# Optimization experiments

Measured on AMD Instinct MI355X. Metric: run time of the kernel, lower is better.

## Reference

```python
import jax, jax.numpy as jnp
import numpy as np
import math

D_MODEL = 1024
NUM_HEADS = 16


def setup_inputs() -> dict:
    key = jax.random.key(0)
    k1, k2, k3 = jax.random.split(key, 3)
    x = jax.random.normal(k1, (4, 2048, D_MODEL), dtype=jnp.float32)
    scale = 1.0 / math.sqrt(D_MODEL)
    W_qkv = jax.random.normal(k2, (3 * D_MODEL, D_MODEL), dtype=jnp.float32) * scale
    W_out = jax.random.normal(k3, (D_MODEL, D_MODEL), dtype=jnp.float32) * scale
    return {"x": x, "W_qkv": W_qkv, "W_out": W_out}


def reference(x, W_qkv, W_out):
    B, S, D = x.shape
    H = NUM_HEADS
    hd = D // H
    qkv = x @ W_qkv.T                      # [B,S,3D]
    q, k, v = jnp.split(qkv, 3, axis=-1)
    # [B,S,D] -> [B,H,S,hd]
    q = q.reshape(B, S, H, hd).transpose(0, 2, 1, 3)
    k = k.reshape(B, S, H, hd).transpose(0, 2, 1, 3)
    v = v.reshape(B, S, H, hd).transpose(0, 2, 1, 3)
    scores = jnp.einsum('bhqd,bhkd->bhqk', q, k) / math.sqrt(hd)
    causal = jnp.tril(jnp.ones((S, S), dtype=bool))
    scores = jnp.where(causal, scores, -jnp.inf)
    w = jax.nn.softmax(scores, axis=-1)
    out = jnp.einsum('bhqk,bhkd->bhqd', w, v)
    out = out.transpose(0, 2, 1, 3).reshape(B, S, D)
    return out @ W_out.T
```

## Files before the change

kernel.cpp:

```cpp
#include <hip/hip_runtime.h>
#include <hip/hip_bf16.h>
#include <stdint.h>


typedef __bf16 bf16_t;
typedef __attribute__((ext_vector_type(8))) __bf16 bf16x8;
typedef __attribute__((ext_vector_type(4))) __bf16 bf16x4;
typedef __attribute__((ext_vector_type(4))) float f32x4;

#define LOG2E 1.44269504088896340736f
#define SCLF (0.125f * LOG2E)
#define MFMA16(a, b, c) __builtin_amdgcn_mfma_f32_16x16x32_bf16(a, b, c, 0, 0, 0)

__device__ __forceinline__ bf16x8 ld8(const bf16_t* p) {
    return *(const bf16x8*)p;
}
__device__ __forceinline__ bf16x8 cvt8(const float* p) {
    f32x4 a = *(const f32x4*)p;
    f32x4 b = *(const f32x4*)(p + 4);
    bf16x8 r;
    r[0] = (bf16_t)a[0]; r[1] = (bf16_t)a[1]; r[2] = (bf16_t)a[2]; r[3] = (bf16_t)a[3];
    r[4] = (bf16_t)b[0]; r[5] = (bf16_t)b[1]; r[6] = (bf16_t)b[2]; r[7] = (bf16_t)b[3];
    return r;
}

__device__ __forceinline__ bool probe_f32_wave(const void* w) {
    const uint16_t* u = (const uint16_t*)w;
    const int lane = threadIdx.x & 63;
    const int e = (u[lane] >> 7) & 0xFF;
    const unsigned long long m = __ballot(e >= 96 && e <= 150);
    return __popcll(m) < 56;
}

__device__ __forceinline__ void gll16(const bf16_t* g, bf16_t* l) {
    __builtin_amdgcn_global_load_lds(
        (const __attribute__((address_space(1))) void*)g,
        (__attribute__((address_space(3))) void*)l, 16, 0, 0);
}

__global__ __launch_bounds__(256) void cvt_big_kernel(
    const void* __restrict__ x, const void* __restrict__ wq,
    bf16_t* __restrict__ xb, bf16_t* __restrict__ wqb)
{
    const int gid = blockIdx.x * 256 + threadIdx.x;
    const void* src;
    bf16_t* dst;
    int off;
    if (gid < 1048576) { src = x;  dst = xb;  off = gid; }
    else               { src = wq; dst = wqb; off = gid - 1048576; }
    const bool f32 = probe_f32_wave(src);
    const bf16x8 v = f32 ? cvt8((const float*)src + (size_t)off * 8)
                         : ld8((const bf16_t*)src + (size_t)off * 8);
    *(bf16x8*)(dst + (size_t)off * 8) = v;
}

__global__ __launch_bounds__(256) void cvt_small_kernel(
    const void* __restrict__ wo, bf16_t* __restrict__ wob)
{
    const int off = blockIdx.x * 256 + threadIdx.x;
    const bool f32 = probe_f32_wave(wo);
    const bf16x8 v = f32 ? cvt8((const float*)wo + (size_t)off * 8)
                         : ld8((const bf16_t*)wo + (size_t)off * 8);
    *(bf16x8*)(wob + (size_t)off * 8) = v;
}

template <int EPI>
__global__ __launch_bounds__(256) void gemm_bt_lds(
    const bf16_t* __restrict__ A, const bf16_t* __restrict__ B,
    void* __restrict__ C, bf16_t* __restrict__ VT,
    int M, int N, int K)
{
    __shared__ __align__(16) bf16_t lsA[128 * 32];
    __shared__ __align__(16) bf16_t lsB[128 * 32];

    const int t    = threadIdx.x;
    const int lane = t & 63;
    const int wid  = t >> 6;
    const int quad = lane >> 4;
    const int l15  = lane & 15;
    const int wm   = (wid & 1) * 64;
    const int wn   = (wid >> 1) * 64;
    const int m0   = blockIdx.y * 128;
    const int n0   = blockIdx.x * 128;

    const bf16_t* Ar = A + (size_t)(m0 + (t >> 2)) * K + (t & 3) * 8;
    const bf16_t* Br = B + (size_t)(n0 + (t >> 2)) * K + (t & 3) * 8;
    bf16_t* la = lsA + t * 8;
    bf16_t* lb = lsB + t * 8;

    f32x4 acc[4][4];
#pragma unroll
    for (int i = 0; i < 4; ++i)
#pragma unroll
        for (int j = 0; j < 4; ++j) acc[i][j] = (f32x4){0.f, 0.f, 0.f, 0.f};

    for (int k0 = 0; k0 < K; k0 += 32) {
        __syncthreads();
        gll16(Ar + k0, la);
        gll16(Ar + (size_t)64 * K + k0, la + 2048);
        gll16(Br + k0, lb);
        gll16(Br + (size_t)64 * K + k0, lb + 2048);
        __syncthreads();

        bf16x8 af[4], bfr[4];
#pragma unroll
        for (int i = 0; i < 4; ++i)
            af[i] = ld8(lsA + (wm + i * 16 + l15) * 32 + quad * 8);
#pragma unroll
        for (int j = 0; j < 4; ++j)
            bfr[j] = ld8(lsB + (wn + j * 16 + l15) * 32 + quad * 8);
#pragma unroll
        for (int i = 0; i < 4; ++i)
#pragma unroll
            for (int j = 0; j < 4; ++j)
                acc[i][j] = MFMA16(af[i], bfr[j], acc[i][j]);
    }

#pragma unroll
    for (int i = 0; i < 4; ++i) {
        const int row = m0 + wm + i * 16 + quad * 4;
#pragma unroll
        for (int j = 0; j < 4; ++j) {
            const int col = n0 + wn + j * 16 + l15;
#pragma unroll
            for (int r = 0; r < 4; ++r) {
                const int rr = row + r;
                if (EPI == 0) {
                    ((float*)C)[(size_t)rr * N + col] = acc[i][j][r];
                } else {
                    const bf16_t v = (bf16_t)acc[i][j][r];
                    if (col < 2048) {
                        ((bf16_t*)C)[(size_t)rr * 2048 + col] = v;
                    } else {
                        const int c2 = col - 2048;
                        const int h = c2 >> 6, d = c2 & 63;
                        const int b = rr >> 11, s = rr & 2047;
                        VT[((size_t)((b << 4) + h) * 64 + d) * 2048 + s] = v;
                    }
                }
            }
        }
    }
}

struct Kfrag { bf16x8 k00, k01, k10, k11; };
struct Vfrag { bf16x8 v0, v1, v2, v3; };

__device__ __forceinline__ Kfrag ldk(const bf16_t* Kbase, int key0) {
    const bf16_t* kp = Kbase + (size_t)key0 * 2048;
    Kfrag f;
    f.k00 = ld8(kp);
    f.k01 = ld8(kp + 32);
    f.k10 = ld8(kp + (size_t)16 * 2048);
    f.k11 = ld8(kp + (size_t)16 * 2048 + 32);
    return f;
}
__device__ __forceinline__ Vfrag ldv(const bf16_t* Vbase, int key0) {
    const bf16_t* vp = Vbase + key0;
    Vfrag f;
    f.v0 = ld8(vp);
    f.v1 = ld8(vp + (size_t)16 * 2048);
    f.v2 = ld8(vp + (size_t)32 * 2048);
    f.v3 = ld8(vp + (size_t)48 * 2048);
    return f;
}

__device__ __forceinline__ bf16x4 expq(f32x4 s, float& lsum) {
    bf16x4 r;
#pragma unroll
    for (int i = 0; i < 4; ++i) {
        const float e = exp2f(s[i] * SCLF);
        r[i] = (bf16_t)e;
        lsum += (float)r[i];
    }
    return r;
}
__device__ __forceinline__ bf16x4 expq_m(f32x4 s, float& lsum, int quad, int l15) {
    bf16x4 r;
#pragma unroll
    for (int i = 0; i < 4; ++i) {
        const float e = (quad * 4 + i <= l15) ? exp2f(s[i] * SCLF) : 0.f;
        r[i] = (bf16_t)e;
        lsum += (float)r[i];
    }
    return r;
}

typedef union { bf16x4 h; int u[2]; } pk2;
typedef union { int u[4]; bf16x8 v; } pk4u;

__device__ __forceinline__ bf16x8 xpose(bf16x4 p0, bf16x4 p1, int s0b, int s1b, bool lowsel) {
    pk2 a, b;
    a.h = p0; b.h = p1;
    const int x0 = __builtin_amdgcn_ds_bpermute(s0b, a.u[0]);
    const int y0 = __builtin_amdgcn_ds_bpermute(s0b, b.u[0]);
    const int x1 = __builtin_amdgcn_ds_bpermute(s0b, a.u[1]);
    const int y1 = __builtin_amdgcn_ds_bpermute(s0b, b.u[1]);
    const int x2 = __builtin_amdgcn_ds_bpermute(s1b, a.u[0]);
    const int y2 = __builtin_amdgcn_ds_bpermute(s1b, b.u[0]);
    const int x3 = __builtin_amdgcn_ds_bpermute(s1b, a.u[1]);
    const int y3 = __builtin_amdgcn_ds_bpermute(s1b, b.u[1]);
    pk4u r;
    r.u[0] = lowsel ? x0 : y0;
    r.u[1] = lowsel ? x1 : y1;
    r.u[2] = lowsel ? x2 : y2;
    r.u[3] = lowsel ? x3 : y3;
    return r.v;
}

template <int DIAG>
__device__ __forceinline__ void qk_phase(
    const Kfrag& kf, int quad, int l15, int s0b, int s1b, bool lowsel,
    const bf16x8& qa0, const bf16x8& qa1, const bf16x8& qb0, const bf16x8& qb1,
    bf16x8& pfa, bf16x8& pfb, float& la, float& lb)
{
    const f32x4 Z = (f32x4){0.f, 0.f, 0.f, 0.f};
    f32x4 s0a = Z, s1a = Z, s0b_ = Z, s1b_ = Z;
    s0a = MFMA16(kf.k00, qa0, s0a); s0a = MFMA16(kf.k01, qa1, s0a);
    s0b_ = MFMA16(kf.k00, qb0, s0b_); s0b_ = MFMA16(kf.k01, qb1, s0b_);
    if (!DIAG) {
        s1a = MFMA16(kf.k10, qa0, s1a); s1a = MFMA16(kf.k11, qa1, s1a);
    }
    s1b_ = MFMA16(kf.k10, qb0, s1b_); s1b_ = MFMA16(kf.k11, qb1, s1b_);

    bf16x4 pa0, pa1, pb0, pb1;
    if (DIAG) {
        pa0 = expq_m(s0a, la, quad, l15);
        pa1 = (bf16x4){(bf16_t)0.f, (bf16_t)0.f, (bf16_t)0.f, (bf16_t)0.f};
        pb0 = expq(s0b_, lb);
        pb1 = expq_m(s1b_, lb, quad, l15);
    } else {
        pa0 = expq(s0a, la); pa1 = expq(s1a, la);
        pb0 = expq(s0b_, lb); pb1 = expq(s1b_, lb);
    }
    pfa = xpose(pa0, pa1, s0b, s1b, lowsel);
    pfb = xpose(pb0, pb1, s0b, s1b, lowsel);
}

__device__ __forceinline__ void pv(
    const bf16x8& pfa, const bf16x8& pfb, const Vfrag& v,
    f32x4 (&oa)[4], f32x4 (&ob)[4])
{
    oa[0] = MFMA16(pfa, v.v0, oa[0]); ob[0] = MFMA16(pfb, v.v0, ob[0]);
    oa[1] = MFMA16(pfa, v.v1, oa[1]); ob[1] = MFMA16(pfb, v.v1, ob[1]);
    oa[2] = MFMA16(pfa, v.v2, oa[2]); ob[2] = MFMA16(pfb, v.v2, ob[2]);
    oa[3] = MFMA16(pfa, v.v3, oa[3]); ob[3] = MFMA16(pfb, v.v3, ob[3]);
}

__global__ __launch_bounds__(256, 4) void attn_kernel(
    const bf16_t* __restrict__ qk, const bf16_t* __restrict__ vt,
    bf16_t* __restrict__ out)
{
    const int t    = threadIdx.x;
    const int wid  = t >> 6;
    const int lane = t & 63;
    const int quad = lane >> 4;
    const int l15  = lane & 15;

    const int bx = blockIdx.x;
    const int u  = bx & 255;
    const int v_ = bx >> 8;
    const int bh = ((u & 15) << 2) | wid;
    const int c  = u >> 4;
    const int bs = (v_ & 1) ? (31 - c) : c;
    const int qt = bs + ((v_ >> 1) << 5);
    const int b  = bh >> 4;
    const int h  = bh & 15;
    const int q0 = qt << 5;

    const int s0b = ((((quad << 1)) & 3) * 16 + l15) << 2;
    const int s1b = ((((quad << 1) + 1) & 3) * 16 + l15) << 2;
    const bool lowsel = quad < 2;

    const bf16_t* Qp = qk + (size_t)(b * 2048 + q0 + l15) * 2048 + h * 64 + quad * 8;
    const bf16x8 qa0 = ld8(Qp);
    const bf16x8 qa1 = ld8(Qp + 32);
    const bf16x8 qb0 = ld8(Qp + (size_t)16 * 2048);
    const bf16x8 qb1 = ld8(Qp + (size_t)16 * 2048 + 32);

    const bf16_t* Kbase = qk + (size_t)(b * 2048 + l15) * 2048 + 1024 + h * 64 + quad * 8;
    const bf16_t* Vbase = vt + ((size_t)bh * 64 + l15) * 2048 + quad * 8;

    f32x4 oa[4], ob[4];
#pragma unroll
    for (int v = 0; v < 4; ++v) {
        oa[v] = (f32x4){0.f, 0.f, 0.f, 0.f};
        ob[v] = (f32x4){0.f, 0.f, 0.f, 0.f};
    }
    float la = 0.f, lb = 0.f;

    Kfrag kc = ldk(Kbase, 0);
    Vfrag vc = ldv(Vbase, 0);
    bf16x8 pfa, pfb;

    if (qt > 0) {
        Kfrag kn = ldk(Kbase, 32);
        qk_phase<0>(kc, quad, l15, s0b, s1b, lowsel,
                    qa0, qa1, qb0, qb1, pfa, pfb, la, lb);
        kc = kn;
        for (int kb = 1; kb < qt; ++kb) {
            Kfrag knn = ldk(Kbase, (kb + 1) << 5);
            Vfrag vn  = ldv(Vbase, kb << 5);
            pv(pfa, pfb, vc, oa, ob);
            qk_phase<0>(kc, quad, l15, s0b, s1b, lowsel,
                        qa0, qa1, qb0, qb1, pfa, pfb, la, lb);
            kc = knn; vc = vn;
        }
        Vfrag vn = ldv(Vbase, qt << 5);
        pv(pfa, pfb, vc, oa, ob);
        qk_phase<1>(kc, quad, l15, s0b, s1b, lowsel,
                    qa0, qa1, qb0, qb1, pfa, pfb, la, lb);
        vc = vn;
    } else {
        qk_phase<1>(kc, quad, l15, s0b, s1b, lowsel,
                    qa0, qa1, qb0, qb1, pfa, pfb, la, lb);
    }
    pv(pfa, pfb, vc, oa, ob);

    la += __shfl_xor(la, 16); la += __shfl_xor(la, 32);
    lb += __shfl_xor(lb, 16); lb += __shfl_xor(lb, 32);
    const float inva = 1.0f / la;
    const float invb = 1.0f / lb;

    const size_t obase = (size_t)(b * 2048 + q0 + quad * 4) * 1024 + h * 64 + l15;
#pragma unroll
    for (int r = 0; r < 4; ++r) {
        const float ia = __shfl(inva, quad * 4 + r);
        const float ib = __shfl(invb, quad * 4 + r);
#pragma unroll
        for (int v = 0; v < 4; ++v) {
            out[obase + (size_t)r * 1024 + v * 16]        = (bf16_t)(oa[v][r] * ia);
            out[obase + (size_t)(16 + r) * 1024 + v * 16] = (bf16_t)(ob[v][r] * ib);
        }
    }
}

__global__ void ws_check_kernel(float* out, int code) {
    if (code != 0 && threadIdx.x == 0) out[0] = (float)code;
}

extern "C" void kernel_launch(void* const* d_in, const int* in_sizes, int n_in,
                              void* d_out, int out_size, void* d_ws, size_t ws_size,
                              hipStream_t stream)
{
    const void* x    = d_in[0];
    const void* wqkv = d_in[1];
    const void* wout = d_in[2];

    bf16_t* qkbuf   = (bf16_t*)d_ws;
    bf16_t* vtbuf   = qkbuf + (size_t)8192 * 2048;
    bf16_t* attnbuf = vtbuf + (size_t)64 * 64 * 2048;
    float*  outp    = (float*)d_out;

    bf16_t* xb  = attnbuf;
    bf16_t* wqb = (bf16_t*)d_out;
    bf16_t* wob = vtbuf;

    const int wsBad = (ws_size < (size_t)64 * 1024 * 1024) ? 512 : 0;

    cvt_big_kernel<<<5632, 256, 0, stream>>>(x, wqkv, xb, wqb);

    gemm_bt_lds<1><<<dim3(24, 64), 256, 0, stream>>>(
        xb, wqb, qkbuf, vtbuf, 8192, 3072, 1024);

    attn_kernel<<<1024, 256, 0, stream>>>(qkbuf, vtbuf, attnbuf);

    cvt_small_kernel<<<512, 256, 0, stream>>>(wout, wob);

    gemm_bt_lds<0><<<dim3(8, 64), 256, 0, stream>>>(
        attnbuf, wob, outp, nullptr, 8192, 1024, 1024);

    ws_check_kernel<<<1, 64, 0, stream>>>(outp, wsBad);
}
```

Measured before the change: 339.2 us.

## Split attention work to 16-row query tiles per wave and swizzle GEMM block order

The attention kernel now gives each wave a 16-row query tile instead of 32 rows. Waves in a block cover different query tiles of the same head rather than different heads, and the grid doubles to 2048 blocks with launch bounds raised to 8 blocks per CU. Diagonal handling gains a third mode for odd tiles. This aims to cut per-wave registers, raise occupancy and balance causal work, but each K/V load now feeds half as much MFMA work. Separately, the GEMM remaps block IDs with an XCD-style stride-8 swizzle to improve L2 locality across chiplets.

```diff
diff --git a/kernel.cpp b/kernel.cpp
--- a/kernel.cpp
+++ b/kernel.cpp
@@ -80,8 +80,13 @@
     const int l15  = lane & 15;
     const int wm   = (wid & 1) * 64;
     const int wn   = (wid >> 1) * 64;
-    const int m0   = blockIdx.y * 128;
-    const int n0   = blockIdx.x * 128;
+
+    const int nbx = gridDim.x;
+    const int nwg = nbx * gridDim.y;
+    const int bid = blockIdx.y * nbx + blockIdx.x;
+    const int sid = (bid & 7) * (nwg >> 3) + (bid >> 3);
+    const int m0  = (sid / nbx) * 128;
+    const int n0  = (sid % nbx) * 128;
 
     const bf16_t* Ar = A + (size_t)(m0 + (t >> 2)) * K + (t & 3) * 8;
     const bf16_t* Br = B + (size_t)(n0 + (t >> 2)) * K + (t & 3) * 8;
@@ -208,46 +213,42 @@
     return r.v;
 }
 
-template <int DIAG>
-__device__ __forceinline__ void qk_phase(
+template <int MODE>
+__device__ __forceinline__ void qk16(
     const Kfrag& kf, int quad, int l15, int s0b, int s1b, bool lowsel,
-    const bf16x8& qa0, const bf16x8& qa1, const bf16x8& qb0, const bf16x8& qb1,
-    bf16x8& pfa, bf16x8& pfb, float& la, float& lb)
+    const bf16x8& qa0, const bf16x8& qa1,
+    bf16x8& pfa, float& la)
 {
     const f32x4 Z = (f32x4){0.f, 0.f, 0.f, 0.f};
-    f32x4 s0a = Z, s1a = Z, s0b_ = Z, s1b_ = Z;
-    s0a = MFMA16(kf.k00, qa0, s0a); s0a = MFMA16(kf.k01, qa1, s0a);
-    s0b_ = MFMA16(kf.k00, qb0, s0b_); s0b_ = MFMA16(kf.k01, qb1, s0b_);
-    if (!DIAG) {
-        s1a = MFMA16(kf.k10, qa0, s1a); s1a = MFMA16(kf.k11, qa1, s1a);
-    }
-    s1b_ = MFMA16(kf.k10, qb0, s1b_); s1b_ = MFMA16(kf.k11, qb1, s1b_);
-
-    bf16x4 pa0, pa1, pb0, pb1;
-    if (DIAG) {
-        pa0 = expq_m(s0a, la, quad, l15);
-        pa1 = (bf16x4){(bf16_t)0.f, (bf16_t)0.f, (bf16_t)0.f, (bf16_t)0.f};
-        pb0 = expq(s0b_, lb);
-        pb1 = expq_m(s1b_, lb, quad, l15);
+    f32x4 s0 = Z, s1 = Z;
+    s0 = MFMA16(kf.k00, qa0, s0); s0 = MFMA16(kf.k01, qa1, s0);
+    if (MODE != 1) {
+        s1 = MFMA16(kf.k10, qa0, s1); s1 = MFMA16(kf.k11, qa1, s1);
+    }
+    bf16x4 p0, p1;
+    if (MODE == 0) {
+        p0 = expq(s0, la);
+        p1 = expq(s1, la);
+    } else if (MODE == 1) {
+        p0 = expq_m(s0, la, quad, l15);
+        p1 = (bf16x4){(bf16_t)0.f, (bf16_t)0.f, (bf16_t)0.f, (bf16_t)0.f};
     } else {
-        pa0 = expq(s0a, la); pa1 = expq(s1a, la);
-        pb0 = expq(s0b_, lb); pb1 = expq(s1b_, lb);
-    }
-    pfa = xpose(pa0, pa1, s0b, s1b, lowsel);
-    pfb = xpose(pb0, pb1, s0b, s1b, lowsel);
-}
-
-__device__ __forceinline__ void pv(
-    const bf16x8& pfa, const bf16x8& pfb, const Vfrag& v,
-    f32x4 (&oa)[4], f32x4 (&ob)[4])
-{
-    oa[0] = MFMA16(pfa, v.v0, oa[0]); ob[0] = MFMA16(pfb, v.v0, ob[0]);
-    oa[1] = MFMA16(pfa, v.v1, oa[1]); ob[1] = MFMA16(pfb, v.v1, ob[1]);
-    oa[2] = MFMA16(pfa, v.v2, oa[2]); ob[2] = MFMA16(pfb, v.v2, ob[2]);
-    oa[3] = MFMA16(pfa, v.v3, oa[3]); ob[3] = MFMA16(pfb, v.v3, ob[3]);
-}
-
-__global__ __launch_bounds__(256, 4) void attn_kernel(
+        p0 = expq(s0, la);
+        p1 = expq_m(s1, la, quad, l15);
+    }
+    pfa = xpose(p0, p1, s0b, s1b, lowsel);
+}
+
+__device__ __forceinline__ void pv16(
+    const bf16x8& pfa, const Vfrag& v, f32x4 (&oa)[4])
+{
+    oa[0] = MFMA16(pfa, v.v0, oa[0]);
+    oa[1] = MFMA16(pfa, v.v1, oa[1]);
+    oa[2] = MFMA16(pfa, v.v2, oa[2]);
+    oa[3] = MFMA16(pfa, v.v3, oa[3]);
+}
+
+__global__ __launch_bounds__(256, 8) void attn_kernel(
     const bf16_t* __restrict__ qk, const bf16_t* __restrict__ vt,
     bf16_t* __restrict__ out)
 {
@@ -260,13 +261,16 @@
     const int bx = blockIdx.x;
     const int u  = bx & 255;
     const int v_ = bx >> 8;
-    const int bh = ((u & 15) << 2) | wid;
+
+    const int bh = ((u & 15) << 2) | (v_ & 3);
     const int c  = u >> 4;
-    const int bs = (v_ & 1) ? (31 - c) : c;
-    const int qt = bs + ((v_ >> 1) << 5);
+    const int vh = v_ >> 2;
+    const int hi = vh ? (7 - wid) : wid;
+    const int cc = (hi & 1) ? (15 - c) : c;
+    const int qt = (hi << 4) | cc;
     const int b  = bh >> 4;
     const int h  = bh & 15;
-    const int q0 = qt << 5;
+    const int q0 = qt << 4;
 
     const int s0b = ((((quad << 1)) & 3) * 16 + l15) << 2;
     const int s1b = ((((quad << 1) + 1) & 3) * 16 + l15) << 2;
@@ -275,63 +279,56 @@
     const bf16_t* Qp = qk + (size_t)(b * 2048 + q0 + l15) * 2048 + h * 64 + quad * 8;
     const bf16x8 qa0 = ld8(Qp);
     const bf16x8 qa1 = ld8(Qp + 32);
-    const bf16x8 qb0 = ld8(Qp + (size_t)16 * 2048);
-    const bf16x8 qb1 = ld8(Qp + (size_t)16 * 2048 + 32);
 
     const bf16_t* Kbase = qk + (size_t)(b * 2048 + l15) * 2048 + 1024 + h * 64 + quad * 8;
     const bf16_t* Vbase = vt + ((size_t)bh * 64 + l15) * 2048 + quad * 8;
 
-    f32x4 oa[4], ob[4];
-#pragma unroll
-    for (int v = 0; v < 4; ++v) {
-        oa[v] = (f32x4){0.f, 0.f, 0.f, 0.f};
-        ob[v] = (f32x4){0.f, 0.f, 0.f, 0.f};
-    }
-    float la = 0.f, lb = 0.f;
-
+    f32x4 oa[4];
+#pragma unroll
+    for (int v = 0; v < 4; ++v) oa[v] = (f32x4){0.f, 0.f, 0.f, 0.f};
+    float la = 0.f;
+
+    const int nkb = (qt >> 1) + 1;
     Kfrag kc = ldk(Kbase, 0);
     Vfrag vc = ldv(Vbase, 0);
-    bf16x8 pfa, pfb;
-
-    if (qt > 0) {
+    bf16x8 pfa;
+
+    if (nkb > 1) {
         Kfrag kn = ldk(Kbase, 32);
-        qk_phase<0>(kc, quad, l15, s0b, s1b, lowsel,
-                    qa0, qa1, qb0, qb1, pfa, pfb, la, lb);
+        qk16<0>(kc, quad, l15, s0b, s1b, lowsel, qa0, qa1, pfa, la);
         kc = kn;
-        for (int kb = 1; kb < qt; ++kb) {
+        for (int kb = 1; kb < nkb - 1; ++kb) {
             Kfrag knn = ldk(Kbase, (kb + 1) << 5);
             Vfrag vn  = ldv(Vbase, kb << 5);
-            pv(pfa, pfb, vc, oa, ob);
-            qk_phase<0>(kc, quad, l15, s0b, s1b, lowsel,
-                        qa0, qa1, qb0, qb1, pfa, pfb, la, lb);
+            pv16(pfa, vc, oa);
+            qk16<0>(kc, quad, l15, s0b, s1b, lowsel, qa0, qa1, pfa, la);
             kc = knn; vc = vn;
         }
-        Vfrag vn = ldv(Vbase, qt << 5);
-        pv(pfa, pfb, vc, oa, ob);
-        qk_phase<1>(kc, quad, l15, s0b, s1b, lowsel,
-                    qa0, qa1, qb0, qb1, pfa, pfb, la, lb);
+        Vfrag vn = ldv(Vbase, (nkb - 1) << 5);
+        pv16(pfa, vc, oa);
+        if (qt & 1)
+            qk16<2>(kc, quad, l15, s0b, s1b, lowsel, qa0, qa1, pfa, la);
+        else
+            qk16<1>(kc, quad, l15, s0b, s1b, lowsel, qa0, qa1, pfa, la);
         vc = vn;
     } else {
-        qk_phase<1>(kc, quad, l15, s0b, s1b, lowsel,
-                    qa0, qa1, qb0, qb1, pfa, pfb, la, lb);
-    }
-    pv(pfa, pfb, vc, oa, ob);
+        if (qt & 1)
+            qk16<2>(kc, quad, l15, s0b, s1b, lowsel, qa0, qa1, pfa, la);
+        else
+            qk16<1>(kc, quad, l15, s0b, s1b, lowsel, qa0, qa1, pfa, la);
+    }
+    pv16(pfa, vc, oa);
 
     la += __shfl_xor(la, 16); la += __shfl_xor(la, 32);
-    lb += __shfl_xor(lb, 16); lb += __shfl_xor(lb, 32);
     const float inva = 1.0f / la;
-    const float invb = 1.0f / lb;
 
     const size_t obase = (size_t)(b * 2048 + q0 + quad * 4) * 1024 + h * 64 + l15;
 #pragma unroll
     for (int r = 0; r < 4; ++r) {
         const float ia = __shfl(inva, quad * 4 + r);
-        const float ib = __shfl(invb, quad * 4 + r);
-#pragma unroll
-        for (int v = 0; v < 4; ++v) {
-            out[obase + (size_t)r * 1024 + v * 16]        = (bf16_t)(oa[v][r] * ia);
-            out[obase + (size_t)(16 + r) * 1024 + v * 16] = (bf16_t)(ob[v][r] * ib);
-        }
+#pragma unroll
+        for (int v = 0; v < 4; ++v)
+            out[obase + (size_t)r * 1024 + v * 16] = (bf16_t)(oa[v][r] * ia);
     }
 }
 
@@ -363,7 +360,7 @@
     gemm_bt_lds<1><<<dim3(24, 64), 256, 0, stream>>>(
         xb, wqb, qkbuf, vtbuf, 8192, 3072, 1024);
 
-    attn_kernel<<<1024, 256, 0, stream>>>(qkbuf, vtbuf, attnbuf);
+    attn_kernel<<<2048, 256, 0, stream>>>(qkbuf, vtbuf, attnbuf);
 
     cvt_small_kernel<<<512, 256, 0, stream>>>(wout, wob);
 
```

Measured after the change: 515.7 us. 1.52x slower.

## Split causal attention KV range in two with merge pass, swizzle GEMM blocks

Applied to the files above, without the earlier changes.

The attention kernel now launches twice as many blocks, each handling half of a query tile's causal key range. Each block writes unnormalized partial outputs and row sums, and a new merge kernel adds the two halves and normalizes. This is meant to shorten the longest per-block chain and improve CU utilization, at the cost of extra partial-buffer traffic and one more launch. The GEMM block index is also remapped with a stride-8 swizzle so neighbouring tiles land on the same XCD, aiming to improve L2 reuse.

```diff
diff --git a/kernel.cpp b/kernel.cpp
--- a/kernel.cpp
+++ b/kernel.cpp
@@ -80,8 +80,13 @@
     const int l15  = lane & 15;
     const int wm   = (wid & 1) * 64;
     const int wn   = (wid >> 1) * 64;
-    const int m0   = blockIdx.y * 128;
-    const int n0   = blockIdx.x * 128;
+
+    const int nbx = gridDim.x;
+    const int nwg = nbx * gridDim.y;
+    const int bid = blockIdx.y * nbx + blockIdx.x;
+    const int sid = (bid & 7) * (nwg >> 3) + (bid >> 3);
+    const int m0  = (sid / nbx) * 128;
+    const int n0  = (sid % nbx) * 128;
 
     const bf16_t* Ar = A + (size_t)(m0 + (t >> 2)) * K + (t & 3) * 8;
     const bf16_t* Br = B + (size_t)(n0 + (t >> 2)) * K + (t & 3) * 8;
@@ -249,7 +254,8 @@
 
 __global__ __launch_bounds__(256, 4) void attn_kernel(
     const bf16_t* __restrict__ qk, const bf16_t* __restrict__ vt,
-    bf16_t* __restrict__ out)
+    bf16_t* __restrict__ p0buf, bf16_t* __restrict__ p1buf,
+    float* __restrict__ lbuf0, float* __restrict__ lbuf1)
 {
     const int t    = threadIdx.x;
     const int wid  = t >> 6;
@@ -262,11 +268,18 @@
     const int v_ = bx >> 8;
     const int bh = ((u & 15) << 2) | wid;
     const int c  = u >> 4;
-    const int bs = (v_ & 1) ? (31 - c) : c;
-    const int qt = bs + ((v_ >> 1) << 5);
+    const int v2 = v_ & 3;
+    const int bs = (v2 & 1) ? (31 - c) : c;
+    const int qt = bs + ((v2 >> 1) << 5);
+    const int half = v_ >> 2;
     const int b  = bh >> 4;
     const int h  = bh & 15;
     const int q0 = qt << 5;
+
+    const int mid = (qt + 1) >> 1;
+    const int lo  = half ? mid : 0;
+    const int hi  = half ? (qt + 1) : mid;
+    const int cnt = hi - lo;
 
     const int s0b = ((((quad << 1)) & 3) * 16 + l15) << 2;
     const int s1b = ((((quad << 1) + 1) & 3) * 16 + l15) << 2;
@@ -289,50 +302,84 @@
     }
     float la = 0.f, lb = 0.f;
 
-    Kfrag kc = ldk(Kbase, 0);
-    Vfrag vc = ldv(Vbase, 0);
-    bf16x8 pfa, pfb;
-
-    if (qt > 0) {
-        Kfrag kn = ldk(Kbase, 32);
-        qk_phase<0>(kc, quad, l15, s0b, s1b, lowsel,
-                    qa0, qa1, qb0, qb1, pfa, pfb, la, lb);
-        kc = kn;
-        for (int kb = 1; kb < qt; ++kb) {
-            Kfrag knn = ldk(Kbase, (kb + 1) << 5);
-            Vfrag vn  = ldv(Vbase, kb << 5);
-            pv(pfa, pfb, vc, oa, ob);
+    if (cnt > 0) {
+        Kfrag kc = ldk(Kbase, lo << 5);
+        Vfrag vc = ldv(Vbase, lo << 5);
+        bf16x8 pfa, pfb;
+
+        if (cnt > 1) {
+            Kfrag kn = ldk(Kbase, (lo + 1) << 5);
             qk_phase<0>(kc, quad, l15, s0b, s1b, lowsel,
                         qa0, qa1, qb0, qb1, pfa, pfb, la, lb);
-            kc = knn; vc = vn;
+            kc = kn;
+            for (int kb = lo + 1; kb < hi - 1; ++kb) {
+                Kfrag knn = ldk(Kbase, (kb + 1) << 5);
+                Vfrag vn  = ldv(Vbase, kb << 5);
+                pv(pfa, pfb, vc, oa, ob);
+                qk_phase<0>(kc, quad, l15, s0b, s1b, lowsel,
+                            qa0, qa1, qb0, qb1, pfa, pfb, la, lb);
+                kc = knn; vc = vn;
+            }
+            Vfrag vn = ldv(Vbase, (hi - 1) << 5);
+            pv(pfa, pfb, vc, oa, ob);
+            if (half)
+                qk_phase<1>(kc, quad, l15, s0b, s1b, lowsel,
+                            qa0, qa1, qb0, qb1, pfa, pfb, la, lb);
+            else
+                qk_phase<0>(kc, quad, l15, s0b, s1b, lowsel,
+                            qa0, qa1, qb0, qb1, pfa, pfb, la, lb);
+            vc = vn;
+        } else {
+            if (lo == qt)
+                qk_phase<1>(kc, quad, l15, s0b, s1b, lowsel,
+                            qa0, qa1, qb0, qb1, pfa, pfb, la, lb);
+            else
+                qk_phase<0>(kc, quad, l15, s0b, s1b, lowsel,
+                            qa0, qa1, qb0, qb1, pfa, pfb, la, lb);
         }
-        Vfrag vn = ldv(Vbase, qt << 5);
         pv(pfa, pfb, vc, oa, ob);
-        qk_phase<1>(kc, quad, l15, s0b, s1b, lowsel,
-                    qa0, qa1, qb0, qb1, pfa, pfb, la, lb);
-        vc = vn;
-    } else {
-        qk_phase<1>(kc, quad, l15, s0b, s1b, lowsel,
-                    qa0, qa1, qb0, qb1, pfa, pfb, la, lb);
-    }
-    pv(pfa, pfb, vc, oa, ob);
+    }
 
     la += __shfl_xor(la, 16); la += __shfl_xor(la, 32);
     lb += __shfl_xor(lb, 16); lb += __shfl_xor(lb, 32);
-    const float inva = 1.0f / la;
-    const float invb = 1.0f / lb;
-
+
+    bf16_t* pb = half ? p1buf : p0buf;
     const size_t obase = (size_t)(b * 2048 + q0 + quad * 4) * 1024 + h * 64 + l15;
 #pragma unroll
     for (int r = 0; r < 4; ++r) {
-        const float ia = __shfl(inva, quad * 4 + r);
-        const float ib = __shfl(invb, quad * 4 + r);
 #pragma unroll
         for (int v = 0; v < 4; ++v) {
-            out[obase + (size_t)r * 1024 + v * 16]        = (bf16_t)(oa[v][r] * ia);
-            out[obase + (size_t)(16 + r) * 1024 + v * 16] = (bf16_t)(ob[v][r] * ib);
+            pb[obase + (size_t)r * 1024 + v * 16]        = (bf16_t)oa[v][r];
+            pb[obase + (size_t)(16 + r) * 1024 + v * 16] = (bf16_t)ob[v][r];
         }
     }
+    float* lf = half ? lbuf1 : lbuf0;
+    if (quad == 0) {
+        lf[(size_t)bh * 2048 + q0 + l15]      = la;
+        lf[(size_t)bh * 2048 + q0 + 16 + l15] = lb;
+    }
+}
+
+__global__ __launch_bounds__(256) void merge_kernel(
+    const bf16_t* __restrict__ p1buf,
+    const float* __restrict__ lbuf0, const float* __restrict__ lbuf1,
+    bf16_t* __restrict__ p0buf)
+{
+    const int gid = blockIdx.x * 256 + threadIdx.x;
+    const size_t e0 = (size_t)gid * 8;
+    const int row = (int)(e0 >> 10);
+    const int col = (int)(e0 & 1023);
+    const int b = row >> 11, s = row & 2047;
+    const int h = col >> 6;
+    const size_t li = (size_t)((b << 4) + h) * 2048 + s;
+    const float inv = 1.0f / (lbuf0[li] + lbuf1[li]);
+    const bf16x8 a = ld8(p0buf + e0);
+    const bf16x8 c = ld8(p1buf + e0);
+    bf16x8 o;
+#pragma unroll
+    for (int i = 0; i < 8; ++i)
+        o[i] = (bf16_t)(((float)a[i] + (float)c[i]) * inv);
+    *(bf16x8*)(p0buf + e0) = o;
 }
 
 __global__ void ws_check_kernel(float* out, int code) {
@@ -352,9 +399,12 @@
     bf16_t* attnbuf = vtbuf + (size_t)64 * 64 * 2048;
     float*  outp    = (float*)d_out;
 
-    bf16_t* xb  = attnbuf;
-    bf16_t* wqb = (bf16_t*)d_out;
-    bf16_t* wob = vtbuf;
+    bf16_t* xb    = attnbuf;
+    bf16_t* wqb   = (bf16_t*)d_out;
+    bf16_t* p1buf = (bf16_t*)d_out;
+    float*  lbuf0 = (float*)((char*)d_out + (size_t)16 * 1024 * 1024);
+    float*  lbuf1 = lbuf0 + (size_t)64 * 2048;
+    bf16_t* wob   = vtbuf;
 
     const int wsBad = (ws_size < (size_t)64 * 1024 * 1024) ? 512 : 0;
 
@@ -363,7 +413,10 @@
     gemm_bt_lds<1><<<dim3(24, 64), 256, 0, stream>>>(
         xb, wqb, qkbuf, vtbuf, 8192, 3072, 1024);
 
-    attn_kernel<<<1024, 256, 0, stream>>>(qkbuf, vtbuf, attnbuf);
+    attn_kernel<<<2048, 256, 0, stream>>>(qkbuf, vtbuf, attnbuf, p1buf,
+                                          lbuf0, lbuf1);
+
+    merge_kernel<<<4096, 256, 0, stream>>>(p1buf, lbuf0, lbuf1, attnbuf);
 
     cvt_small_kernel<<<512, 256, 0, stream>>>(wout, wob);
 
```

After: 364.4 us. +7.4%, slower.

## Deepen GEMM K-step to 64, swizzle block order, vectorize V-transpose stores

Applied to the files above, without the earlier changes.

The GEMM kernel now stages a 64-wide K slice per barrier pair, using twice the LDS, which halves the number of synchronizations per tile. Workgroup IDs are remapped with a stride-8 swizzle so that blocks landing on the same XCD share A/B tiles in cache. The transposed V epilogue packs four consecutive sequence elements into a single bf16x4 store instead of four scalar stores. The larger LDS footprint may reduce occupancy, and the swizzle assumes the number of workgroups is divisible by 8.

```diff
diff --git a/kernel.cpp b/kernel.cpp
--- a/kernel.cpp
+++ b/kernel.cpp
@@ -70,8 +70,8 @@
     void* __restrict__ C, bf16_t* __restrict__ VT,
     int M, int N, int K)
 {
-    __shared__ __align__(16) bf16_t lsA[128 * 32];
-    __shared__ __align__(16) bf16_t lsB[128 * 32];
+    __shared__ __align__(16) bf16_t lsA[2 * 128 * 32];
+    __shared__ __align__(16) bf16_t lsB[2 * 128 * 32];
 
     const int t    = threadIdx.x;
     const int lane = t & 63;
@@ -80,13 +80,13 @@
     const int l15  = lane & 15;
     const int wm   = (wid & 1) * 64;
     const int wn   = (wid >> 1) * 64;
-    const int m0   = blockIdx.y * 128;
-    const int n0   = blockIdx.x * 128;
-
-    const bf16_t* Ar = A + (size_t)(m0 + (t >> 2)) * K + (t & 3) * 8;
-    const bf16_t* Br = B + (size_t)(n0 + (t >> 2)) * K + (t & 3) * 8;
-    bf16_t* la = lsA + t * 8;
-    bf16_t* lb = lsB + t * 8;
+
+    const int nbx = gridDim.x;
+    const int nwg = nbx * gridDim.y;
+    const int bid = blockIdx.y * nbx + blockIdx.x;
+    const int sid = (bid & 7) * (nwg >> 3) + (bid >> 3);
+    const int m0  = (sid / nbx) * 128;
+    const int n0  = (sid % nbx) * 128;
 
     f32x4 acc[4][4];
 #pragma unroll
@@ -94,26 +94,32 @@
 #pragma unroll
         for (int j = 0; j < 4; ++j) acc[i][j] = (f32x4){0.f, 0.f, 0.f, 0.f};
 
-    for (int k0 = 0; k0 < K; k0 += 32) {
+    for (int k0 = 0; k0 < K; k0 += 64) {
         __syncthreads();
-        gll16(Ar + k0, la);
-        gll16(Ar + (size_t)64 * K + k0, la + 2048);
-        gll16(Br + k0, lb);
-        gll16(Br + (size_t)64 * K + k0, lb + 2048);
+#pragma unroll
+        for (int j = 0; j < 4; ++j) {
+            const int row = (j & 1) * 64 + (t >> 2);
+            const int col = k0 + (j >> 1) * 32 + (t & 3) * 8;
+            gll16(A + (size_t)(m0 + row) * K + col, lsA + j * 2048 + t * 8);
+            gll16(B + (size_t)(n0 + row) * K + col, lsB + j * 2048 + t * 8);
+        }
         __syncthreads();
 
-        bf16x8 af[4], bfr[4];
-#pragma unroll
-        for (int i = 0; i < 4; ++i)
-            af[i] = ld8(lsA + (wm + i * 16 + l15) * 32 + quad * 8);
-#pragma unroll
-        for (int j = 0; j < 4; ++j)
-            bfr[j] = ld8(lsB + (wn + j * 16 + l15) * 32 + quad * 8);
-#pragma unroll
-        for (int i = 0; i < 4; ++i)
+#pragma unroll 1
+        for (int h = 0; h < 2; ++h) {
+            bf16x8 af[4], bfr[4];
+#pragma unroll
+            for (int i = 0; i < 4; ++i)
+                af[i] = ld8(lsA + h * 4096 + (wm + i * 16 + l15) * 32 + quad * 8);
 #pragma unroll
             for (int j = 0; j < 4; ++j)
-                acc[i][j] = MFMA16(af[i], bfr[j], acc[i][j]);
+                bfr[j] = ld8(lsB + h * 4096 + (wn + j * 16 + l15) * 32 + quad * 8);
+#pragma unroll
+            for (int i = 0; i < 4; ++i)
+#pragma unroll
+                for (int j = 0; j < 4; ++j)
+                    acc[i][j] = MFMA16(af[i], bfr[j], acc[i][j]);
+        }
     }
 
 #pragma unroll
@@ -122,22 +128,22 @@
 #pragma unroll
         for (int j = 0; j < 4; ++j) {
             const int col = n0 + wn + j * 16 + l15;
-#pragma unroll
-            for (int r = 0; r < 4; ++r) {
-                const int rr = row + r;
-                if (EPI == 0) {
-                    ((float*)C)[(size_t)rr * N + col] = acc[i][j][r];
-                } else {
-                    const bf16_t v = (bf16_t)acc[i][j][r];
-                    if (col < 2048) {
-                        ((bf16_t*)C)[(size_t)rr * 2048 + col] = v;
-                    } else {
-                        const int c2 = col - 2048;
-                        const int h = c2 >> 6, d = c2 & 63;
-                        const int b = rr >> 11, s = rr & 2047;
-                        VT[((size_t)((b << 4) + h) * 64 + d) * 2048 + s] = v;
-                    }
-                }
+            if (EPI == 0) {
+#pragma unroll
+                for (int r = 0; r < 4; ++r)
+                    ((float*)C)[(size_t)(row + r) * N + col] = acc[i][j][r];
+            } else if (col < 2048) {
+#pragma unroll
+                for (int r = 0; r < 4; ++r)
+                    ((bf16_t*)C)[(size_t)(row + r) * 2048 + col] = (bf16_t)acc[i][j][r];
+            } else {
+                const int c2 = col - 2048;
+                const int h = c2 >> 6, d = c2 & 63;
+                const int b = row >> 11, s = row & 2047;
+                bf16x4 pk;
+#pragma unroll
+                for (int r = 0; r < 4; ++r) pk[r] = (bf16_t)acc[i][j][r];
+                *(bf16x4*)(VT + ((size_t)((b << 4) + h) * 64 + d) * 2048 + s) = pk;
             }
         }
     }
```

Result: faster. 304.6 us (-10.2%).
